# Performance work log

Hardware: AMD Instinct MI355X
Metric: run time of the kernel (lower is better)

The kernel has to match this reference:

```python
import jax, jax.numpy as jnp
import numpy as np

B, H, W, C = 4, 64, 64, 512
DQK = C // 8


def setup_inputs() -> dict:
    key = jax.random.key(0)
    k1, k2, k3, k4 = jax.random.split(key, 4)
    x = jax.random.normal(k1, (B, H, W, C), dtype=jnp.float32)
    kernel_f = jax.random.normal(k2, (1, 1, C, DQK), dtype=jnp.float32) * 0.02
    kernel_g = jax.random.normal(k3, (1, 1, C, DQK), dtype=jnp.float32) * 0.02
    kernel_h = jax.random.normal(k4, (1, 1, C, C), dtype=jnp.float32) * 0.02
    gamma = jnp.ones((1,), dtype=jnp.float32)  # nonzero so attention branch contributes
    return {"x": x, "kernel_f": kernel_f, "kernel_g": kernel_g,
            "kernel_h": kernel_h, "gamma": gamma}


def reference(x, kernel_f, kernel_g, kernel_h, gamma):
    b, h, w, c = x.shape
    n = h * w
    xt = x.reshape(b, n, c)  # 1x1 conv == per-pixel matmul
    f = jnp.einsum('bnc,cd->bnd', xt, kernel_f[0, 0])       # [b,n,dqk]
    g = jnp.einsum('bnc,cd->bnd', xt, kernel_g[0, 0])       # [b,n,dqk]
    v = jnp.einsum('bnc,cd->bnd', xt, kernel_h[0, 0])       # [b,n,c]
    s = jnp.einsum('bid,bjd->bij', f, g)                    # [b,n,n] = f @ g^T
    beta = jax.nn.softmax(s, axis=-1)
    out = jnp.einsum('bij,bjc->bic', beta, v)               # [b,n,c]
    out = out.reshape(b, h, w, c)
    return gamma * out + x
```

## Files before the change

kernel.cpp:

```cpp
#include <hip/hip_runtime.h>


typedef __bf16 bf16x8 __attribute__((ext_vector_type(8)));
typedef __bf16 bf16x2 __attribute__((ext_vector_type(2)));
typedef float f32x4 __attribute__((ext_vector_type(4)));
typedef unsigned int u32x4 __attribute__((ext_vector_type(4)));
typedef unsigned int u32;

#define L2E 1.4426950408889634f

__device__ __forceinline__ unsigned short f2bf(float f) {
    unsigned int u = __builtin_bit_cast(unsigned int, f);
    u += 0x7fffu + ((u >> 16) & 1u);
    return (unsigned short)(u >> 16);
}
__device__ __forceinline__ u32 cvtpk(float a, float b) {
    bf16x2 t; t[0] = (__bf16)a; t[1] = (__bf16)b;
    return __builtin_bit_cast(u32, t);
}
__device__ __forceinline__ bf16x8 ld8(const void* p) {
    u32x4 u = *reinterpret_cast<const u32x4*>(p);
    return __builtin_bit_cast(bf16x8, u);
}
__device__ __forceinline__ bf16x8 ldx(const float* p) {
    float4 a = *reinterpret_cast<const float4*>(p);
    float4 b = *reinterpret_cast<const float4*>(p + 4);
    u32x4 r;
    r.x = cvtpk(a.x, a.y); r.y = cvtpk(a.z, a.w);
    r.z = cvtpk(b.x, b.y); r.w = cvtpk(b.z, b.w);
    return __builtin_bit_cast(bf16x8, r);
}
__device__ __forceinline__ f32x4 mfma16(bf16x8 a, bf16x8 b, f32x4 c) {
    return __builtin_amdgcn_mfma_f32_16x16x32_bf16(a, b, c, 0, 0, 0);
}
__device__ __forceinline__ void gl2lds16(const void* g, void* l) {
    __builtin_amdgcn_global_load_lds(
        (const __attribute__((address_space(1))) u32*)g,
        (__attribute__((address_space(3))) u32*)l, 16, 0, 0);
}

__global__ __launch_bounds__(256) void cvt_w_all(const float* __restrict__ kf,
                                                 const float* __restrict__ kg,
                                                 const float* __restrict__ kh,
                                                 unsigned short* __restrict__ wst) {
    int idx = blockIdx.x * 256 + threadIdx.x;
    int j = idx & 7;
    int gi = idx >> 3;
    int c = gi % 640;
    int sq = gi / 640;
    int k = (sq >> 2) * 32 + (sq & 3) * 8 + j;
    float v;
    if (c < 64)       v = kf[k * 64 + c] * L2E;
    else if (c < 128) v = kg[k * 64 + (c - 64)];
    else              v = kh[k * 512 + (c - 128)];
    wst[idx] = f2bf(v);
}

__global__ __launch_bounds__(256, 2) void proj_k(const float* __restrict__ x,
                                                 const unsigned short* __restrict__ wst,
                                                 unsigned short* __restrict__ fq,
                                                 unsigned short* __restrict__ kst,
                                                 unsigned short* __restrict__ vst) {
    __shared__ __align__(16) unsigned char Wl[2][20480];
    __shared__ unsigned short Tl[64][72];

    int m0 = blockIdx.x * 64;
    int grp = blockIdx.y;
    int tid = threadIdx.x;
    int w = tid >> 6, l = tid & 63, g = l >> 4, i = l & 15;

    const char* wsrc = (const char*)wst + (size_t)w * 10240 + (size_t)grp * 5120 + l * 16;

#pragma unroll
    for (int s5 = 0; s5 < 5; s5++)
        gl2lds16(wsrc + s5 * 1024, &Wl[0][w * 5120 + s5 * 1024]);

    const float* xrow = x + (size_t)(m0 + 16 * w + i) * 512 + g * 8;
    bf16x8 af[16];
#pragma unroll
    for (int k = 0; k < 16; k++) af[k] = ldx(xrow + 32 * k);

    f32x4 acc[5][4];
#pragma unroll
    for (int t = 0; t < 5; t++)
#pragma unroll
        for (int cf = 0; cf < 4; cf++) acc[t][cf] = f32x4{0, 0, 0, 0};

    int rdoff = g * 5120 + i * 16;

#pragma unroll
    for (int q = 0; q < 16; q++) {
        __syncthreads();
        if (q < 15) {
            const char* src = wsrc + (size_t)(q + 1) * 40960;
#pragma unroll
            for (int s5 = 0; s5 < 5; s5++)
                gl2lds16(src + s5 * 1024, &Wl[(q + 1) & 1][w * 5120 + s5 * 1024]);
        }
        const unsigned char* Wb = &Wl[q & 1][0];
        __builtin_amdgcn_s_setprio(1);
#pragma unroll
        for (int t = 0; t < 5; t++)
#pragma unroll
            for (int cf = 0; cf < 4; cf++) {
                bf16x8 bb = ld8(Wb + rdoff + (t * 64 + 16 * cf) * 16);
                acc[t][cf] = mfma16(af[q], bb, acc[t][cf]);
            }
        __builtin_amdgcn_s_setprio(0);
    }

    int batch = m0 >> 12;
    int kt = (m0 & 4095) >> 6;
    unsigned short* kbase = kst + (size_t)batch * 262144 + (size_t)kt * 4096;
    unsigned short* vbase = vst + (size_t)batch * 2097152 + (size_t)kt * 32768;

#pragma unroll
    for (int t = 0; t < 5; t++) {
        if (grp == 0 && t == 0) {
#pragma unroll
            for (int cf = 0; cf < 4; cf++)
#pragma unroll
                for (int r = 0; r < 4; r++)
                    fq[(size_t)(m0 + 16 * w + 4 * g + r) * 64 + 16 * cf + i] =
                        f2bf(acc[t][cf][r]);
        } else {
            __syncthreads();
#pragma unroll
            for (int cf = 0; cf < 4; cf++) {
                ushort4 v4;
                v4.x = f2bf(acc[t][cf][0]); v4.y = f2bf(acc[t][cf][1]);
                v4.z = f2bf(acc[t][cf][2]); v4.w = f2bf(acc[t][cf][3]);
                *reinterpret_cast<ushort4*>(&Tl[16 * cf + i][16 * w + 4 * g]) = v4;
            }
            __syncthreads();
            if (grp == 0 && t == 1) {
#pragma unroll
                for (int ch = tid; ch < 512; ch += 256) {
                    int jf2 = ch >> 7, ks = (ch >> 6) & 1, l2 = ch & 63;
                    int g2 = l2 >> 4, i2 = l2 & 15;
                    ushort4 o0, o1;
                    o0.x = Tl[ks * 32 + 8 * g2 + 0][16 * jf2 + i2];
                    o0.y = Tl[ks * 32 + 8 * g2 + 1][16 * jf2 + i2];
                    o0.z = Tl[ks * 32 + 8 * g2 + 2][16 * jf2 + i2];
                    o0.w = Tl[ks * 32 + 8 * g2 + 3][16 * jf2 + i2];
                    o1.x = Tl[ks * 32 + 8 * g2 + 4][16 * jf2 + i2];
                    o1.y = Tl[ks * 32 + 8 * g2 + 5][16 * jf2 + i2];
                    o1.z = Tl[ks * 32 + 8 * g2 + 6][16 * jf2 + i2];
                    o1.w = Tl[ks * 32 + 8 * g2 + 7][16 * jf2 + i2];
                    unsigned short* dst = kbase + (size_t)(jf2 * 1024 + ks * 512 + l2 * 8);
                    *reinterpret_cast<ushort4*>(dst)     = o0;
                    *reinterpret_cast<ushort4*>(dst + 4) = o1;
                }
            } else {
                int n0 = (grp == 0) ? (t - 2) * 64 : 192 + t * 64;
#pragma unroll
                for (int ch = tid; ch < 512; ch += 256) {
                    int cc = ch >> 7, ks = (ch >> 6) & 1, l2 = ch & 63;
                    int g2 = l2 >> 4, i2 = l2 & 15;
                    int row = cc * 16 + i2;
                    int jb = 32 * ks + 4 * g2;
                    ushort4 o0, o1;
                    o0.x = Tl[row][jb + 0];  o0.y = Tl[row][jb + 1];
                    o0.z = Tl[row][jb + 2];  o0.w = Tl[row][jb + 3];
                    o1.x = Tl[row][jb + 16]; o1.y = Tl[row][jb + 17];
                    o1.z = Tl[row][jb + 18]; o1.w = Tl[row][jb + 19];
                    int c16 = (n0 >> 4) + cc;
                    unsigned short* dst = vbase + (size_t)(c16 * 1024 + ks * 512 + l2 * 8);
                    *reinterpret_cast<ushort4*>(dst)     = o0;
                    *reinterpret_cast<ushort4*>(dst + 4) = o1;
                }
            }
        }
    }
}

__global__ __launch_bounds__(512, 2) void attn_k(const unsigned short* __restrict__ fq,
                                                 const unsigned short* __restrict__ kst,
                                                 const unsigned short* __restrict__ vst,
                                                 const float* __restrict__ x,
                                                 const float* __restrict__ gamma,
                                                 float* __restrict__ out) {
    __shared__ __align__(16) unsigned char Pl[2][8192];
    __shared__ float l_lds[64];

    int bid = blockIdx.x;
    int xcd = bid & 7;
    int batch = xcd >> 1;
    int qidx = ((xcd & 1) << 5) | (bid >> 3);
    int q0 = qidx * 64;

    int tid = threadIdx.x;
    int w = tid >> 6, l = tid & 63, g = l >> 4, i = l & 15;
    int jf = w >> 1, qfh = w & 1;

    if (tid < 64) l_lds[tid] = 0.0f;

    const unsigned short* fqb = fq + (size_t)batch * 4096 * 64;
    const char* kb = (const char*)kst + (size_t)batch * 524288;
    const char* vb = (const char*)vst + (size_t)batch * 4194304;

    bf16x8 aQ[2][2];
#pragma unroll
    for (int qf_l = 0; qf_l < 2; qf_l++)
#pragma unroll
        for (int ks = 0; ks < 2; ks++)
            aQ[qf_l][ks] = ld8(fqb + (size_t)(q0 + 16 * (2 * qfh + qf_l) + i) * 64 +
                               ks * 32 + g * 8);

    f32x4 acc[4][4];
#pragma unroll
    for (int a = 0; a < 4; a++)
#pragma unroll
        for (int b = 0; b < 4; b++) acc[a][b] = f32x4{0, 0, 0, 0};
    float lp[2] = {0.0f, 0.0f};

    bf16x8 kA[2];
#pragma unroll
    for (int ks = 0; ks < 2; ks++)
        kA[ks] = ld8(kb + (size_t)jf * 2048 + ks * 1024 + l * 16);

    int pwoff = ((2 * qfh) * 2 + (jf >> 1)) * 1024 + l * 16 + (jf & 1) * 8;

    for (int t = 0; t < 64; ++t) {
        bf16x8 vB[4][2];
#pragma unroll
        for (int cf = 0; cf < 4; cf++)
#pragma unroll
            for (int ks = 0; ks < 2; ks++)
                vB[cf][ks] = ld8(vb + (size_t)(t * 32 + w * 4 + cf) * 2048 +
                                 ks * 1024 + l * 16);

        f32x4 sacc[2] = {f32x4{0,0,0,0}, f32x4{0,0,0,0}};
#pragma unroll
        for (int qf_l = 0; qf_l < 2; qf_l++) {
            sacc[qf_l] = mfma16(kA[0], aQ[qf_l][0], sacc[qf_l]);
            sacc[qf_l] = mfma16(kA[1], aQ[qf_l][1], sacc[qf_l]);
        }

        {
            int tn = (t + 1) & 63;
            const char* kn = kb + (size_t)(tn * 4 + jf) * 2048;
            kA[0] = ld8(kn + l * 16);
            kA[1] = ld8(kn + 1024 + l * 16);
        }

        unsigned char* Pb = &Pl[t & 1][0];
#pragma unroll
        for (int qf_l = 0; qf_l < 2; qf_l++) {
            float p0 = __builtin_amdgcn_exp2f(sacc[qf_l][0]);
            float p1 = __builtin_amdgcn_exp2f(sacc[qf_l][1]);
            float p2 = __builtin_amdgcn_exp2f(sacc[qf_l][2]);
            float p3 = __builtin_amdgcn_exp2f(sacc[qf_l][3]);
            lp[qf_l] += (p0 + p1) + (p2 + p3);
            uint2 pk2;
            pk2.x = cvtpk(p0, p1);
            pk2.y = cvtpk(p2, p3);
            *reinterpret_cast<uint2*>(Pb + pwoff + qf_l * 2048) = pk2;
        }

        __syncthreads();

        const unsigned char* Pr = &Pl[t & 1][0];
        bf16x8 aP[4][2];
#pragma unroll
        for (int qf = 0; qf < 4; qf++)
#pragma unroll
            for (int ks = 0; ks < 2; ks++)
                aP[qf][ks] = ld8(Pr + (qf * 2 + ks) * 1024 + l * 16);

        __builtin_amdgcn_s_setprio(1);
#pragma unroll
        for (int cf = 0; cf < 4; cf++)
#pragma unroll
            for (int qf = 0; qf < 4; qf++) {
                acc[qf][cf] = mfma16(aP[qf][0], vB[cf][0], acc[qf][cf]);
                acc[qf][cf] = mfma16(aP[qf][1], vB[cf][1], acc[qf][cf]);
            }
        __builtin_amdgcn_s_setprio(0);
    }

#pragma unroll
    for (int qf_l = 0; qf_l < 2; qf_l++) {
        lp[qf_l] += __shfl_xor(lp[qf_l], 16, 64);
        lp[qf_l] += __shfl_xor(lp[qf_l], 32, 64);
    }
    if (g == 0) {
        atomicAdd(&l_lds[16 * (2 * qfh + 0) + i], lp[0]);
        atomicAdd(&l_lds[16 * (2 * qfh + 1) + i], lp[1]);
    }
    __syncthreads();

    float gam = gamma[0];
#pragma unroll
    for (int qf = 0; qf < 4; qf++) {
#pragma unroll
        for (int r = 0; r < 4; r++) {
            float linv = gam / l_lds[16 * qf + 4 * g + r];
            int n = q0 + 16 * qf + 4 * g + r;
            size_t base = ((size_t)batch * 4096 + n) * 512 + 64 * w;
#pragma unroll
            for (int cf = 0; cf < 4; cf++)
                out[base + 16 * cf + i] = acc[qf][cf][r] * linv + x[base + 16 * cf + i];
        }
    }
}


extern "C" void kernel_launch(void* const* d_in, const int* in_sizes, int n_in,
                              void* d_out, int out_size, void* d_ws, size_t ws_size,
                              hipStream_t stream) {
    const float* x = (const float*)d_in[0];
    const float* kf = (const float*)d_in[1];
    const float* kg = (const float*)d_in[2];
    const float* kh = (const float*)d_in[3];
    const float* gamma = (const float*)d_in[4];
    float* out = (float*)d_out;

    char* ws = (char*)d_ws;
    unsigned short* Fq  = (unsigned short*)(ws);
    unsigned short* Kst = (unsigned short*)(ws + 2097152);
    unsigned short* Vst = (unsigned short*)(ws + 4194304);
    unsigned short* Wst = (unsigned short*)(ws + 20971520);

    cvt_w_all<<<1280, 256, 0, stream>>>(kf, kg, kh, Wst);
    proj_k<<<dim3(256, 2), 256, 0, stream>>>(x, Wst, Fq, Kst, Vst);
    attn_k<<<256, 512, 0, stream>>>(Fq, Kst, Vst, x, gamma, out);
}
```

Before: 120.2 us.

## Software-pipeline QK scores one tile ahead of PV accumulation

Restructures the attention loop so the score MFMA, exp2 and P write for tile t+1 are issued alongside the PV MFMAs of tile t. A prologue computes the first tile, K loads are prefetched two tiles ahead, and the V loads now sit after the barrier. The aim is to hide exp/LDS-write latency behind the matrix work and keep the MFMA pipe busy. In exchange it does one extra wasted score computation on the last iteration, masked out of the row sum, and keeps more registers live.

```diff
diff --git a/kernel.cpp b/kernel.cpp
--- a/kernel.cpp
+++ b/kernel.cpp
@@ -214,37 +214,20 @@
         for (int b = 0; b < 4; b++) acc[a][b] = f32x4{0, 0, 0, 0};
     float lp[2] = {0.0f, 0.0f};
 
+    int pwoff = ((2 * qfh) * 2 + (jf >> 1)) * 1024 + l * 16 + (jf & 1) * 8;
+
     bf16x8 kA[2];
-#pragma unroll
-    for (int ks = 0; ks < 2; ks++)
-        kA[ks] = ld8(kb + (size_t)jf * 2048 + ks * 1024 + l * 16);
-
-    int pwoff = ((2 * qfh) * 2 + (jf >> 1)) * 1024 + l * 16 + (jf & 1) * 8;
-
-    for (int t = 0; t < 64; ++t) {
-        bf16x8 vB[4][2];
-#pragma unroll
-        for (int cf = 0; cf < 4; cf++)
-#pragma unroll
-            for (int ks = 0; ks < 2; ks++)
-                vB[cf][ks] = ld8(vb + (size_t)(t * 32 + w * 4 + cf) * 2048 +
-                                 ks * 1024 + l * 16);
-
+    kA[0] = ld8(kb + (size_t)jf * 2048 + l * 16);
+    kA[1] = ld8(kb + (size_t)jf * 2048 + 1024 + l * 16);
+    {
         f32x4 sacc[2] = {f32x4{0,0,0,0}, f32x4{0,0,0,0}};
 #pragma unroll
         for (int qf_l = 0; qf_l < 2; qf_l++) {
             sacc[qf_l] = mfma16(kA[0], aQ[qf_l][0], sacc[qf_l]);
             sacc[qf_l] = mfma16(kA[1], aQ[qf_l][1], sacc[qf_l]);
         }
-
-        {
-            int tn = (t + 1) & 63;
-            const char* kn = kb + (size_t)(tn * 4 + jf) * 2048;
-            kA[0] = ld8(kn + l * 16);
-            kA[1] = ld8(kn + 1024 + l * 16);
-        }
-
-        unsigned char* Pb = &Pl[t & 1][0];
+        kA[0] = ld8(kb + (size_t)(4 + jf) * 2048 + l * 16);
+        kA[1] = ld8(kb + (size_t)(4 + jf) * 2048 + 1024 + l * 16);
 #pragma unroll
         for (int qf_l = 0; qf_l < 2; qf_l++) {
             float p0 = __builtin_amdgcn_exp2f(sacc[qf_l][0]);
@@ -255,10 +238,20 @@
             uint2 pk2;
             pk2.x = cvtpk(p0, p1);
             pk2.y = cvtpk(p2, p3);
-            *reinterpret_cast<uint2*>(Pb + pwoff + qf_l * 2048) = pk2;
-        }
-
+            *reinterpret_cast<uint2*>(&Pl[0][0] + pwoff + qf_l * 2048) = pk2;
+        }
+    }
+
+    for (int t = 0; t < 64; ++t) {
         __syncthreads();
+
+        bf16x8 vB[4][2];
+#pragma unroll
+        for (int cf = 0; cf < 4; cf++)
+#pragma unroll
+            for (int ks = 0; ks < 2; ks++)
+                vB[cf][ks] = ld8(vb + (size_t)(t * 32 + w * 4 + cf) * 2048 +
+                                 ks * 1024 + l * 16);
 
         const unsigned char* Pr = &Pl[t & 1][0];
         bf16x8 aP[4][2];
@@ -267,6 +260,20 @@
 #pragma unroll
             for (int ks = 0; ks < 2; ks++)
                 aP[qf][ks] = ld8(Pr + (qf * 2 + ks) * 1024 + l * 16);
+
+        f32x4 sacc[2] = {f32x4{0,0,0,0}, f32x4{0,0,0,0}};
+#pragma unroll
+        for (int qf_l = 0; qf_l < 2; qf_l++) {
+            sacc[qf_l] = mfma16(kA[0], aQ[qf_l][0], sacc[qf_l]);
+            sacc[qf_l] = mfma16(kA[1], aQ[qf_l][1], sacc[qf_l]);
+        }
+
+        {
+            int tk = (t + 2) & 63;
+            const char* kn = kb + (size_t)(tk * 4 + jf) * 2048;
+            kA[0] = ld8(kn + l * 16);
+            kA[1] = ld8(kn + 1024 + l * 16);
+        }
 
         __builtin_amdgcn_s_setprio(1);
 #pragma unroll
@@ -277,6 +284,21 @@
                 acc[qf][cf] = mfma16(aP[qf][1], vB[cf][1], acc[qf][cf]);
             }
         __builtin_amdgcn_s_setprio(0);
+
+        float msk = (t < 63) ? 1.0f : 0.0f;
+        unsigned char* Pb = &Pl[(t + 1) & 1][0];
+#pragma unroll
+        for (int qf_l = 0; qf_l < 2; qf_l++) {
+            float p0 = __builtin_amdgcn_exp2f(sacc[qf_l][0]);
+            float p1 = __builtin_amdgcn_exp2f(sacc[qf_l][1]);
+            float p2 = __builtin_amdgcn_exp2f(sacc[qf_l][2]);
+            float p3 = __builtin_amdgcn_exp2f(sacc[qf_l][3]);
+            lp[qf_l] += msk * ((p0 + p1) + (p2 + p3));
+            uint2 pk2;
+            pk2.x = cvtpk(p0, p1);
+            pk2.y = cvtpk(p2, p3);
+            *reinterpret_cast<uint2*>(Pb + pwoff + qf_l * 2048) = pk2;
+        }
     }
 
 #pragma unroll
```

Result: faster. 116.8 us (-2.8%).

## Software-pipeline attention loop two tiles deep with one barrier per pair

Applied to the files above, without the earlier changes.

Restructures the main attention loop to process two key tiles per iteration. The QK^T MFMA and softmax exp for the next pair now overlap with the PV MFMAs of the current pair. V and K fragments are prefetched one stage ahead into double register sets, and the P buffer in LDS grows to four slots. This halves the number of barriers and hides global-load and exp latency, at the cost of more registers and LDS, which may reduce occupancy. The last iteration computes wrapped-around tiles and masks their contribution to the row sum.

```diff
diff --git a/kernel.cpp b/kernel.cpp
--- a/kernel.cpp
+++ b/kernel.cpp
@@ -180,7 +180,7 @@
                                                  const float* __restrict__ x,
                                                  const float* __restrict__ gamma,
                                                  float* __restrict__ out) {
-    __shared__ __align__(16) unsigned char Pl[2][8192];
+    __shared__ __align__(16) unsigned char Pl[4][8192];
     __shared__ float l_lds[64];
 
     int bid = blockIdx.x;
@@ -214,69 +214,158 @@
         for (int b = 0; b < 4; b++) acc[a][b] = f32x4{0, 0, 0, 0};
     float lp[2] = {0.0f, 0.0f};
 
-    bf16x8 kA[2];
-#pragma unroll
-    for (int ks = 0; ks < 2; ks++)
-        kA[ks] = ld8(kb + (size_t)jf * 2048 + ks * 1024 + l * 16);
-
     int pwoff = ((2 * qfh) * 2 + (jf >> 1)) * 1024 + l * 16 + (jf & 1) * 8;
-
-    for (int t = 0; t < 64; ++t) {
-        bf16x8 vB[4][2];
-#pragma unroll
-        for (int cf = 0; cf < 4; cf++)
-#pragma unroll
-            for (int ks = 0; ks < 2; ks++)
-                vB[cf][ks] = ld8(vb + (size_t)(t * 32 + w * 4 + cf) * 2048 +
-                                 ks * 1024 + l * 16);
-
-        f32x4 sacc[2] = {f32x4{0,0,0,0}, f32x4{0,0,0,0}};
+    int c16w = w * 4;
+
+    bf16x8 kAa[2], kAb[2];
+    kAa[0] = ld8(kb + (size_t)jf * 2048 + l * 16);
+    kAa[1] = ld8(kb + (size_t)jf * 2048 + 1024 + l * 16);
+    kAb[0] = ld8(kb + (size_t)(4 + jf) * 2048 + l * 16);
+    kAb[1] = ld8(kb + (size_t)(4 + jf) * 2048 + 1024 + l * 16);
+
+    bf16x8 vbr_a[4][2], vbr_b[4][2];
+#pragma unroll
+    for (int cf = 0; cf < 4; cf++)
+#pragma unroll
+        for (int ks = 0; ks < 2; ks++) {
+            vbr_a[cf][ks] = ld8(vb + (size_t)(c16w + cf) * 2048 + ks * 1024 + l * 16);
+            vbr_b[cf][ks] = ld8(vb + (size_t)(32 + c16w + cf) * 2048 + ks * 1024 + l * 16);
+        }
+
+    {
+        f32x4 s0[2] = {f32x4{0,0,0,0}, f32x4{0,0,0,0}};
+        f32x4 s1[2] = {f32x4{0,0,0,0}, f32x4{0,0,0,0}};
 #pragma unroll
         for (int qf_l = 0; qf_l < 2; qf_l++) {
-            sacc[qf_l] = mfma16(kA[0], aQ[qf_l][0], sacc[qf_l]);
-            sacc[qf_l] = mfma16(kA[1], aQ[qf_l][1], sacc[qf_l]);
+            s0[qf_l] = mfma16(kAa[0], aQ[qf_l][0], s0[qf_l]);
+            s0[qf_l] = mfma16(kAa[1], aQ[qf_l][1], s0[qf_l]);
+            s1[qf_l] = mfma16(kAb[0], aQ[qf_l][0], s1[qf_l]);
+            s1[qf_l] = mfma16(kAb[1], aQ[qf_l][1], s1[qf_l]);
+        }
+        kAa[0] = ld8(kb + (size_t)(8 + jf) * 2048 + l * 16);
+        kAa[1] = ld8(kb + (size_t)(8 + jf) * 2048 + 1024 + l * 16);
+        kAb[0] = ld8(kb + (size_t)(12 + jf) * 2048 + l * 16);
+        kAb[1] = ld8(kb + (size_t)(12 + jf) * 2048 + 1024 + l * 16);
+#pragma unroll
+        for (int qf_l = 0; qf_l < 2; qf_l++) {
+            float p0 = __builtin_amdgcn_exp2f(s0[qf_l][0]);
+            float p1 = __builtin_amdgcn_exp2f(s0[qf_l][1]);
+            float p2 = __builtin_amdgcn_exp2f(s0[qf_l][2]);
+            float p3 = __builtin_amdgcn_exp2f(s0[qf_l][3]);
+            lp[qf_l] += (p0 + p1) + (p2 + p3);
+            uint2 pk2; pk2.x = cvtpk(p0, p1); pk2.y = cvtpk(p2, p3);
+            *reinterpret_cast<uint2*>(&Pl[0][0] + pwoff + qf_l * 2048) = pk2;
+            p0 = __builtin_amdgcn_exp2f(s1[qf_l][0]);
+            p1 = __builtin_amdgcn_exp2f(s1[qf_l][1]);
+            p2 = __builtin_amdgcn_exp2f(s1[qf_l][2]);
+            p3 = __builtin_amdgcn_exp2f(s1[qf_l][3]);
+            lp[qf_l] += (p0 + p1) + (p2 + p3);
+            pk2.x = cvtpk(p0, p1); pk2.y = cvtpk(p2, p3);
+            *reinterpret_cast<uint2*>(&Pl[1][0] + pwoff + qf_l * 2048) = pk2;
+        }
+    }
+
+    for (int u = 0; u < 32; ++u) {
+        asm volatile("s_waitcnt lgkmcnt(0)" ::: "memory");
+        __builtin_amdgcn_s_barrier();
+
+        const unsigned char* Pr0 = &Pl[(u & 1) * 2][0];
+        const unsigned char* Pr1 = Pr0 + 8192;
+
+        f32x4 s0[2] = {f32x4{0,0,0,0}, f32x4{0,0,0,0}};
+        f32x4 s1[2] = {f32x4{0,0,0,0}, f32x4{0,0,0,0}};
+#pragma unroll
+        for (int qf_l = 0; qf_l < 2; qf_l++) {
+            s0[qf_l] = mfma16(kAa[0], aQ[qf_l][0], s0[qf_l]);
+            s0[qf_l] = mfma16(kAa[1], aQ[qf_l][1], s0[qf_l]);
+            s1[qf_l] = mfma16(kAb[0], aQ[qf_l][0], s1[qf_l]);
+            s1[qf_l] = mfma16(kAb[1], aQ[qf_l][1], s1[qf_l]);
         }
 
         {
-            int tn = (t + 1) & 63;
-            const char* kn = kb + (size_t)(tn * 4 + jf) * 2048;
-            kA[0] = ld8(kn + l * 16);
-            kA[1] = ld8(kn + 1024 + l * 16);
-        }
-
-        unsigned char* Pb = &Pl[t & 1][0];
+            int ta = (2 * u + 4) & 63, tb = (2 * u + 5) & 63;
+            const char* ka = kb + (size_t)(ta * 4 + jf) * 2048;
+            const char* kp = kb + (size_t)(tb * 4 + jf) * 2048;
+            kAa[0] = ld8(ka + l * 16);
+            kAa[1] = ld8(ka + 1024 + l * 16);
+            kAb[0] = ld8(kp + l * 16);
+            kAb[1] = ld8(kp + 1024 + l * 16);
+        }
+
+        {
+            bf16x8 aP[4][2];
+#pragma unroll
+            for (int qf = 0; qf < 4; qf++)
+#pragma unroll
+                for (int ks = 0; ks < 2; ks++)
+                    aP[qf][ks] = ld8(Pr0 + (qf * 2 + ks) * 1024 + l * 16);
+            __builtin_amdgcn_s_setprio(1);
+#pragma unroll
+            for (int cf = 0; cf < 4; cf++)
+#pragma unroll
+                for (int qf = 0; qf < 4; qf++) {
+                    acc[qf][cf] = mfma16(aP[qf][0], vbr_a[cf][0], acc[qf][cf]);
+                    acc[qf][cf] = mfma16(aP[qf][1], vbr_a[cf][1], acc[qf][cf]);
+                }
+            __builtin_amdgcn_s_setprio(0);
+        }
+        {
+            int tv = (2 * u + 2) & 63;
+#pragma unroll
+            for (int cf = 0; cf < 4; cf++)
+#pragma unroll
+                for (int ks = 0; ks < 2; ks++)
+                    vbr_a[cf][ks] = ld8(vb + (size_t)(tv * 32 + c16w + cf) * 2048 +
+                                        ks * 1024 + l * 16);
+        }
+
+        {
+            bf16x8 aP[4][2];
+#pragma unroll
+            for (int qf = 0; qf < 4; qf++)
+#pragma unroll
+                for (int ks = 0; ks < 2; ks++)
+                    aP[qf][ks] = ld8(Pr1 + (qf * 2 + ks) * 1024 + l * 16);
+            __builtin_amdgcn_s_setprio(1);
+#pragma unroll
+            for (int cf = 0; cf < 4; cf++)
+#pragma unroll
+                for (int qf = 0; qf < 4; qf++) {
+                    acc[qf][cf] = mfma16(aP[qf][0], vbr_b[cf][0], acc[qf][cf]);
+                    acc[qf][cf] = mfma16(aP[qf][1], vbr_b[cf][1], acc[qf][cf]);
+                }
+            __builtin_amdgcn_s_setprio(0);
+        }
+        {
+            int tv = (2 * u + 3) & 63;
+#pragma unroll
+            for (int cf = 0; cf < 4; cf++)
+#pragma unroll
+                for (int ks = 0; ks < 2; ks++)
+                    vbr_b[cf][ks] = ld8(vb + (size_t)(tv * 32 + c16w + cf) * 2048 +
+                                        ks * 1024 + l * 16);
+        }
+
+        float msk = (u < 31) ? 1.0f : 0.0f;
+        unsigned char* Pw0 = &Pl[((u + 1) & 1) * 2][0];
+        unsigned char* Pw1 = Pw0 + 8192;
 #pragma unroll
         for (int qf_l = 0; qf_l < 2; qf_l++) {
-            float p0 = __builtin_amdgcn_exp2f(sacc[qf_l][0]);
-            float p1 = __builtin_amdgcn_exp2f(sacc[qf_l][1]);
-            float p2 = __builtin_amdgcn_exp2f(sacc[qf_l][2]);
-            float p3 = __builtin_amdgcn_exp2f(sacc[qf_l][3]);
-            lp[qf_l] += (p0 + p1) + (p2 + p3);
-            uint2 pk2;
-            pk2.x = cvtpk(p0, p1);
-            pk2.y = cvtpk(p2, p3);
-            *reinterpret_cast<uint2*>(Pb + pwoff + qf_l * 2048) = pk2;
-        }
-
-        __syncthreads();
-
-        const unsigned char* Pr = &Pl[t & 1][0];
-        bf16x8 aP[4][2];
-#pragma unroll
-        for (int qf = 0; qf < 4; qf++)
-#pragma unroll
-            for (int ks = 0; ks < 2; ks++)
-                aP[qf][ks] = ld8(Pr + (qf * 2 + ks) * 1024 + l * 16);
-
-        __builtin_amdgcn_s_setprio(1);
-#pragma unroll
-        for (int cf = 0; cf < 4; cf++)
-#pragma unroll
-            for (int qf = 0; qf < 4; qf++) {
-                acc[qf][cf] = mfma16(aP[qf][0], vB[cf][0], acc[qf][cf]);
-                acc[qf][cf] = mfma16(aP[qf][1], vB[cf][1], acc[qf][cf]);
-            }
-        __builtin_amdgcn_s_setprio(0);
+            float p0 = __builtin_amdgcn_exp2f(s0[qf_l][0]);
+            float p1 = __builtin_amdgcn_exp2f(s0[qf_l][1]);
+            float p2 = __builtin_amdgcn_exp2f(s0[qf_l][2]);
+            float p3 = __builtin_amdgcn_exp2f(s0[qf_l][3]);
+            lp[qf_l] += msk * ((p0 + p1) + (p2 + p3));
+            uint2 pk2; pk2.x = cvtpk(p0, p1); pk2.y = cvtpk(p2, p3);
+            *reinterpret_cast<uint2*>(Pw0 + pwoff + qf_l * 2048) = pk2;
+            p0 = __builtin_amdgcn_exp2f(s1[qf_l][0]);
+            p1 = __builtin_amdgcn_exp2f(s1[qf_l][1]);
+            p2 = __builtin_amdgcn_exp2f(s1[qf_l][2]);
+            p3 = __builtin_amdgcn_exp2f(s1[qf_l][3]);
+            lp[qf_l] += msk * ((p0 + p1) + (p2 + p3));
+            pk2.x = cvtpk(p0, p1); pk2.y = cvtpk(p2, p3);
+            *reinterpret_cast<uint2*>(Pw1 + pwoff + qf_l * 2048) = pk2;
+        }
     }
 
 #pragma unroll
```

New measurement: 109.8 us, median of 2. -8.7%, faster.
